# Kernel optimization log

Hardware: AMD Instinct MI355X
Metric: run time of the kernel (lower is better)

## Reference

```python
import jax, jax.numpy as jnp
import numpy as np

EPS = 1e-5
NUM_HEADS = 16
NUM_KV_HEADS = 4
HEAD_DIM = 64
TOP_K = 2


def _layer_norm(x, w, b):
    m = jnp.mean(x, axis=-1, keepdims=True)
    v = jnp.mean((x - m) ** 2, axis=-1, keepdims=True)
    return (x - m) * jax.lax.rsqrt(v + EPS) * w + b


def setup_inputs() -> dict:
    key = jax.random.key(0)
    ks = jax.random.split(key, 8)
    S, B, H = 2048, 1, 1024
    E, F = 8, 4096
    q_per_kv = NUM_HEADS // NUM_KV_HEADS
    qkv_out = NUM_KV_HEADS * (q_per_kv + 2) * HEAD_DIM  # 1536

    def w(k, shape, scale=0.02):
        return jax.random.normal(k, shape, dtype=jnp.float32) * scale

    return {
        "hidden_states": jax.random.normal(ks[0], (S, B, H), dtype=jnp.float32),
        "ln1_weight": jnp.ones((H,), jnp.float32),
        "ln1_bias": jnp.zeros((H,), jnp.float32),
        "ln2_weight": jnp.ones((H,), jnp.float32),
        "ln2_bias": jnp.zeros((H,), jnp.float32),
        "qkv_weight": w(ks[1], (qkv_out, H)),
        "proj_weight": w(ks[2], (H, H)),
        "router_weight": w(ks[3], (H, E)),
        "moe_w1": w(ks[4], (E, H, F)),
        "moe_w2": w(ks[5], (E, F, H)),
    }


def reference(hidden_states, ln1_weight, ln1_bias, ln2_weight, ln2_bias,
              qkv_weight, proj_weight, router_weight, moe_w1, moe_w2):
    S, B, H = hidden_states.shape
    D = HEAD_DIM
    Hq, Hkv = NUM_HEADS, NUM_KV_HEADS
    g = Hq // Hkv                      # queries per kv head (GQA group)
    scale = 1.0 / np.sqrt(D)

    # ---- attention block ----
    ln1_out = _layer_norm(hidden_states, ln1_weight, ln1_bias)
    qkv = ln1_out @ qkv_weight.T                      # [S,B,Hkv*(g+2)*D]
    qkv = qkv.reshape(S, B, Hkv, (g + 2) * D)
    q = qkv[..., : g * D].reshape(S, B, Hq, D)        # [S,B,Hq,D]
    k = qkv[..., g * D : (g + 1) * D]                 # [S,B,Hkv,D]
    v = qkv[..., (g + 1) * D :]                       # [S,B,Hkv,D]

    # cp_size == 1 -> Ulysses all-to-alls are identity
    q_bf = q.transpose(1, 2, 0, 3).reshape(B, Hkv, g, S, D)  # [B,Hkv,g,S,D]
    k_bf = k.transpose(1, 2, 0, 3)                           # [B,Hkv,S,D]
    v_bf = v.transpose(1, 2, 0, 3)

    scores = jnp.einsum("bkgsd,bktd->bkgst", q_bf, k_bf) * scale
    causal = jnp.tril(jnp.ones((S, S), dtype=bool))
    scores = jnp.where(causal, scores, jnp.float32(-1e30))
    probs = jax.nn.softmax(scores, axis=-1)
    attn = jnp.einsum("bkgst,bktd->bkgsd", probs, v_bf)      # [B,Hkv,g,S,D]
    attn = attn.reshape(B, Hq, S, D).transpose(2, 0, 1, 3).reshape(S, B, Hq * D)

    proj_out = attn @ proj_weight.T
    hidden_after_attn = hidden_states + proj_out

    # ---- MoE block ----
    ln2_out = _layer_norm(hidden_after_attn, ln2_weight, ln2_bias)
    x = ln2_out.reshape(-1, H)                        # [T,H]
    T = x.shape[0]

    logits = x @ router_weight                        # [T,E] (fp32)
    rprobs = jax.nn.softmax(logits, axis=-1)
    top_p, top_i = jax.lax.top_k(rprobs, TOP_K)       # [T,k]
    top_p = top_p / jnp.sum(top_p, axis=-1, keepdims=True)

    # ep_size == 1: dispatch/sort/all-to-all are a pure permutation; compute
    # each expert densely over all tokens, then gather the routed outputs
    # (identical math to sort+grouped-GEMM+unsort).
    fc1 = jnp.einsum("th,ehf->etf", x, moe_w1)        # [E,T,F]
    act = jax.nn.gelu(fc1, approximate=False)
    y = jnp.einsum("etf,efh->eth", act, moe_w2)       # [E,T,H]

    tok = jnp.arange(T)[:, None]                      # [T,1]
    gathered = y[top_i, tok, :]                       # [T,k,H]
    moe_out = jnp.sum(gathered * top_p[..., None], axis=1)  # [T,H]

    return hidden_after_attn + moe_out.reshape(S, B, H)
```

## Files before the change

kernel.cpp:

```cpp
#include <hip/hip_runtime.h>
#include <cstdint>
#include <cstddef>

typedef unsigned short u16;
typedef __attribute__((ext_vector_type(8))) short bf16x8;
typedef __attribute__((ext_vector_type(4))) float f32x4;

#define MFMA16(a, b, c) __builtin_amdgcn_mfma_f32_16x16x32_bf16((a), (b), (c), 0, 0, 0)

__device__ __forceinline__ u16 f2bf(float f) {
  uint32_t u = __builtin_bit_cast(uint32_t, f);
  u += 0x7fffu + ((u >> 16) & 1u);
  return (u16)(u >> 16);
}
__device__ __forceinline__ float bf2f(u16 h) {
  uint32_t u = ((uint32_t)h) << 16;
  return __builtin_bit_cast(float, u);
}

__device__ __forceinline__ void gload_lds16(const void* g, void* l) {
  __builtin_amdgcn_global_load_lds(
      (const __attribute__((address_space(1))) uint32_t*)g,
      (__attribute__((address_space(3))) uint32_t*)l, 16, 0, 0);
}

template<bool WRITE_LO, bool WRITE_F32>
__launch_bounds__(256)
__global__ void ln_kernel(const float* __restrict__ in,
                          const float* __restrict__ w, const float* __restrict__ b,
                          u16* __restrict__ out_hi, u16* __restrict__ out_lo,
                          float* __restrict__ out_f32)
{
  int row = blockIdx.x;
  int tid = threadIdx.x;
  const float* x = in + (size_t)row * 1024;
  float4 v = *(const float4*)(x + tid * 4);
  float s  = v.x + v.y + v.z + v.w;
  float s2 = v.x*v.x + v.y*v.y + v.z*v.z + v.w*v.w;
  #pragma unroll
  for (int d = 1; d < 64; d <<= 1) { s += __shfl_xor(s, d); s2 += __shfl_xor(s2, d); }
  __shared__ float red[2][4];
  int wid = tid >> 6;
  if ((tid & 63) == 0) { red[0][wid] = s; red[1][wid] = s2; }
  __syncthreads();
  s  = red[0][0] + red[0][1] + red[0][2] + red[0][3];
  s2 = red[1][0] + red[1][1] + red[1][2] + red[1][3];
  float mean = s * (1.0f / 1024.0f);
  float var  = s2 * (1.0f / 1024.0f) - mean * mean;
  float rstd = rsqrtf(var + 1e-5f);
  float vv[4] = {v.x, v.y, v.z, v.w};
  #pragma unroll
  for (int j = 0; j < 4; ++j) {
    int c = tid * 4 + j;
    float y = (vv[j] - mean) * rstd * w[c] + b[c];
    size_t idx = (size_t)row * 1024 + c;
    u16 hb = f2bf(y);
    out_hi[idx] = hb;
    if (WRITE_LO)  out_lo[idx] = f2bf(y - bf2f(hb));
    if (WRITE_F32) out_f32[idx] = y;
  }
}

__global__ void convert_split_kernel(const float* __restrict__ in,
                                     u16* __restrict__ hi, u16* __restrict__ lo, int n4)
{
  int i = blockIdx.x * blockDim.x + threadIdx.x;
  if (i >= n4) return;
  float4 v = *(const float4*)(in + (size_t)i * 4);
  float a[4] = {v.x, v.y, v.z, v.w};
  u16 hh[4], ll[4];
  #pragma unroll
  for (int j = 0; j < 4; ++j) {
    hh[j] = f2bf(a[j]);
    ll[j] = f2bf(a[j] - bf2f(hh[j]));
  }
  uint2 hp, lp;
  hp.x = (uint32_t)hh[0] | ((uint32_t)hh[1] << 16);
  hp.y = (uint32_t)hh[2] | ((uint32_t)hh[3] << 16);
  lp.x = (uint32_t)ll[0] | ((uint32_t)ll[1] << 16);
  lp.y = (uint32_t)ll[2] | ((uint32_t)ll[3] << 16);
  *(uint2*)(hi + (size_t)i * 4) = hp;
  *(uint2*)(lo + (size_t)i * 4) = lp;
}

__global__ void transpose_convert_kernel(const float* __restrict__ in, u16* __restrict__ out,
                                         int R, int C)
{
  __shared__ float t[32][33];
  size_t ebase = (size_t)blockIdx.z * R * C;
  int c0 = blockIdx.x * 32, r0 = blockIdx.y * 32;
  int tx = threadIdx.x, ty = threadIdx.y;
  #pragma unroll
  for (int i = 0; i < 4; ++i)
    t[ty + 8*i][tx] = in[ebase + (size_t)(r0 + ty + 8*i) * C + (c0 + tx)];
  __syncthreads();
  #pragma unroll
  for (int i = 0; i < 4; ++i)
    out[ebase + (size_t)(c0 + ty + 8*i) * R + (r0 + tx)] = f2bf(t[tx][ty + 8*i]);
}

__global__ void vtrans_kernel(const u16* __restrict__ qkv, u16* __restrict__ vT)
{
  __shared__ u16 t[32][34];
  int kvh = blockIdx.z;
  int s0 = blockIdx.x * 32, d0 = blockIdx.y * 32;
  int tx = threadIdx.x, ty = threadIdx.y;
  #pragma unroll
  for (int i = 0; i < 4; ++i)
    t[ty + 8*i][tx] = qkv[(size_t)(s0 + ty + 8*i) * 1536 + kvh * 384 + 320 + d0 + tx];
  __syncthreads();
  #pragma unroll
  for (int i = 0; i < 4; ++i)
    vT[((size_t)kvh * 64 + d0 + ty + 8*i) * 2048 + (s0 + tx)] = t[tx][ty + 8*i];
}

template<int MODE, bool SPLIT>
__launch_bounds__(256, SPLIT ? 2 : 4)
__global__ void gemm_kernel(const u16* __restrict__ Ahi, const u16* __restrict__ Alo,
                            const u16* __restrict__ Bhi, const u16* __restrict__ Blo,
                            int N, int K,
                            u16* __restrict__ Cb_hi, u16* __restrict__ Cb_lo,
                            float* __restrict__ Cf, const float* __restrict__ resid,
                            const int* __restrict__ tok_of_pair,
                            const int* __restrict__ counts, const int* __restrict__ prefix)
{
  int bn = blockIdx.x, bm = blockIdx.y;
  int row_base = 0;
  int count = 1 << 30;
  int kbeg = 0, kend = K;
  if constexpr (MODE >= 2) {
    int e = blockIdx.z;
    count = counts[e];
    if (bm * 128 >= count) return;
    row_base = prefix[e];
    Bhi += (size_t)e * N * K;
  }
  if constexpr (MODE == 3) {
    int s = bn >> 3;
    bn &= 7;
    int kc = K >> 2;
    kbeg = s * kc; kend = kbeg + kc;
    Cf += (size_t)s * 4096 * 1024;
  }
  __shared__ u16 As[2][SPLIT ? 2 : 1][128 * 32];
  __shared__ u16 Bs[2][SPLIT ? 2 : 1][128 * 32];

  int tid = threadIdx.x;
  int lane = tid & 63;
  int lo16 = lane & 15, hi4 = lane >> 4;
  int wid = tid >> 6, wr = wid >> 1, wc = wid & 1;

  const u16* gA[2][2];
  const u16* gB[2][2];
  int eidx[2];
  #pragma unroll
  for (int q = 0; q < 2; ++q) {
    int el = (q * 256 + tid) * 8;
    int r = el >> 5, c = el & 31;
    eidx[q] = el;
    if constexpr (MODE == 2) {
      int lim = count - bm * 128 - 1;
      int lr = r < lim ? r : lim;
      int token = tok_of_pair[row_base + bm * 128 + lr];
      gA[q][0] = Ahi + (size_t)token * K + c;
    } else if constexpr (MODE == 3) {
      int lim = count - bm * 128 - 1;
      int lr = r < lim ? r : lim;
      gA[q][0] = Ahi + (size_t)(row_base + bm * 128 + lr) * K + c;
    } else {
      gA[q][0] = Ahi + (size_t)(bm * 128 + r) * K + c;
      if constexpr (SPLIT) gA[q][1] = Alo + (size_t)(bm * 128 + r) * K + c;
    }
    gB[q][0] = Bhi + (size_t)(bn * 128 + r) * K + c;
    if constexpr (SPLIT) gB[q][1] = Blo + (size_t)(bn * 128 + r) * K + c;
  }

  auto stage = [&](int buf, int k0) {
    #pragma unroll
    for (int q = 0; q < 2; ++q) {
      gload_lds16(gA[q][0] + k0, &As[buf][0][eidx[q]]);
      gload_lds16(gB[q][0] + k0, &Bs[buf][0][eidx[q]]);
      if constexpr (SPLIT) {
        gload_lds16(gA[q][1] + k0, &As[buf][1][eidx[q]]);
        gload_lds16(gB[q][1] + k0, &Bs[buf][1][eidx[q]]);
      }
    }
  };

  const f32x4 zf = {0.f, 0.f, 0.f, 0.f};
  f32x4 acc[4][4];
  #pragma unroll
  for (int m = 0; m < 4; ++m)
    #pragma unroll
    for (int n = 0; n < 4; ++n) acc[m][n] = zf;

  stage(0, kbeg);
  __syncthreads();

  int cur = 0;
  for (int k0 = kbeg; k0 < kend; k0 += 32, cur ^= 1) {
    if (k0 + 32 < kend) stage(cur ^ 1, k0 + 32);

    bf16x8 a0[4], b0[4], a1[4], b1[4];
    #pragma unroll
    for (int m = 0; m < 4; ++m)
      a0[m] = *(const bf16x8*)&As[cur][0][(wr * 64 + m * 16 + lo16) * 32 + hi4 * 8];
    #pragma unroll
    for (int n = 0; n < 4; ++n)
      b0[n] = *(const bf16x8*)&Bs[cur][0][(wc * 64 + n * 16 + lo16) * 32 + hi4 * 8];
    if constexpr (SPLIT) {
      #pragma unroll
      for (int m = 0; m < 4; ++m)
        a1[m] = *(const bf16x8*)&As[cur][1][(wr * 64 + m * 16 + lo16) * 32 + hi4 * 8];
      #pragma unroll
      for (int n = 0; n < 4; ++n)
        b1[n] = *(const bf16x8*)&Bs[cur][1][(wc * 64 + n * 16 + lo16) * 32 + hi4 * 8];
    }
    #pragma unroll
    for (int m = 0; m < 4; ++m)
      #pragma unroll
      for (int n = 0; n < 4; ++n) {
        acc[m][n] = MFMA16(a0[m], b0[n], acc[m][n]);
        if constexpr (SPLIT) {
          acc[m][n] = MFMA16(a0[m], b1[n], acc[m][n]);
          acc[m][n] = MFMA16(a1[m], b0[n], acc[m][n]);
        }
      }
    __syncthreads();
  }

  #pragma unroll
  for (int m = 0; m < 4; ++m)
    #pragma unroll
    for (int n = 0; n < 4; ++n)
      #pragma unroll
      for (int r = 0; r < 4; ++r) {
        int lr = wr * 64 + m * 16 + hi4 * 4 + r;
        int col = bn * 128 + wc * 64 + n * 16 + lo16;
        float v = acc[m][n][r];
        if constexpr (MODE == 0) {
          size_t idx = (size_t)(bm * 128 + lr) * N + col;
          u16 hb = f2bf(v);
          Cb_hi[idx] = hb;
          Cb_lo[idx] = f2bf(v - bf2f(hb));
        } else if constexpr (MODE == 1) {
          size_t idx = (size_t)(bm * 128 + lr) * N + col;
          Cf[idx] = v + resid[idx];
        } else if constexpr (MODE == 2) {
          if (bm * 128 + lr < count) {
            size_t idx = (size_t)(row_base + bm * 128 + lr) * N + col;
            float g = 0.5f * v * (1.0f + erff(v * 0.70710678118654752f));
            Cb_hi[idx] = f2bf(g);
          }
        } else {
          if (bm * 128 + lr < count) {
            size_t idx = (size_t)(row_base + bm * 128 + lr) * N + col;
            Cf[idx] = v;
          }
        }
      }
}

struct QState {
  bf16x8 qf[2][2];
  f32x4 o[4];
  float m_r[4], l_r[4];
  int qrow[4];
};

__device__ __forceinline__ void qstate_init(QState& S,
    const u16* qkv_hi, const u16* qkv_lo, int q0w, int qoff, int lo16, int hi4)
{
  const u16* ph = qkv_hi + (size_t)(q0w + lo16) * 1536 + qoff + hi4 * 8;
  const u16* pl = qkv_lo + (size_t)(q0w + lo16) * 1536 + qoff + hi4 * 8;
  S.qf[0][0] = *(const bf16x8*)ph;  S.qf[0][1] = *(const bf16x8*)(ph + 32);
  S.qf[1][0] = *(const bf16x8*)pl;  S.qf[1][1] = *(const bf16x8*)(pl + 32);
  const f32x4 zf = {0.f, 0.f, 0.f, 0.f};
  #pragma unroll
  for (int r = 0; r < 4; ++r) { S.m_r[r] = -INFINITY; S.l_r[r] = 0.f; S.qrow[r] = q0w + hi4 * 4 + r; }
  #pragma unroll
  for (int n = 0; n < 4; ++n) S.o[n] = zf;
}

__device__ __forceinline__ void attn_tile(QState& S, int kv0,
    const u16* Ks0, const u16* Ks1, const u16* Vs0, const u16* Vs1,
    u16* Ps0, u16* Ps1, int lo16, int hi4)
{
  const f32x4 zf = {0.f, 0.f, 0.f, 0.f};
  f32x4 sc[4];
  __builtin_amdgcn_s_setprio(1);
  #pragma unroll
  for (int c2 = 0; c2 < 4; ++c2) {
    sc[c2] = zf;
    int krow = c2 * 16 + lo16;
    const u16* kb  = &Ks0[krow * 64];
    const u16* kbl = &Ks1[krow * 64];
    bf16x8 kh0 = *(const bf16x8*)&kb [((hi4    ) ^ (krow & 7)) * 8];
    bf16x8 kh1 = *(const bf16x8*)&kb [((hi4 + 4) ^ (krow & 7)) * 8];
    bf16x8 kl0 = *(const bf16x8*)&kbl[((hi4    ) ^ (krow & 7)) * 8];
    bf16x8 kl1 = *(const bf16x8*)&kbl[((hi4 + 4) ^ (krow & 7)) * 8];
    sc[c2] = MFMA16(S.qf[0][0], kh0, sc[c2]);
    sc[c2] = MFMA16(S.qf[0][1], kh1, sc[c2]);
    sc[c2] = MFMA16(S.qf[0][0], kl0, sc[c2]);
    sc[c2] = MFMA16(S.qf[0][1], kl1, sc[c2]);
    sc[c2] = MFMA16(S.qf[1][0], kh0, sc[c2]);
    sc[c2] = MFMA16(S.qf[1][1], kh1, sc[c2]);
  }
  __builtin_amdgcn_s_setprio(0);

  float tmax[4] = {-INFINITY, -INFINITY, -INFINITY, -INFINITY};
  #pragma unroll
  for (int c2 = 0; c2 < 4; ++c2) {
    int kv = kv0 + c2 * 16 + lo16;
    #pragma unroll
    for (int r = 0; r < 4; ++r) {
      float sv = sc[c2][r] * 0.125f;
      if (kv > S.qrow[r]) sv = -1e30f;
      sc[c2][r] = sv;
      tmax[r] = fmaxf(tmax[r], sv);
    }
  }
  #pragma unroll
  for (int d = 1; d < 16; d <<= 1)
    #pragma unroll
    for (int r = 0; r < 4; ++r)
      tmax[r] = fmaxf(tmax[r], __shfl_xor(tmax[r], d));
  float rs[4], rowsum[4];
  #pragma unroll
  for (int r = 0; r < 4; ++r) {
    float mn = fmaxf(S.m_r[r], tmax[r]);
    rs[r] = __expf(S.m_r[r] - mn);
    S.m_r[r] = mn;
    rowsum[r] = 0.f;
  }
  #pragma unroll
  for (int c2 = 0; c2 < 4; ++c2)
    #pragma unroll
    for (int r = 0; r < 4; ++r) {
      float pv = __expf(sc[c2][r] - S.m_r[r]);
      sc[c2][r] = pv;
      rowsum[r] += pv;
    }
  #pragma unroll
  for (int d = 1; d < 16; d <<= 1)
    #pragma unroll
    for (int r = 0; r < 4; ++r)
      rowsum[r] += __shfl_xor(rowsum[r], d);
  #pragma unroll
  for (int r = 0; r < 4; ++r) S.l_r[r] = S.l_r[r] * rs[r] + rowsum[r];
  #pragma unroll
  for (int n = 0; n < 4; ++n)
    #pragma unroll
    for (int r = 0; r < 4; ++r) S.o[n][r] *= rs[r];

  #pragma unroll
  for (int c2 = 0; c2 < 4; ++c2)
    #pragma unroll
    for (int r = 0; r < 4; ++r) {
      float pv = sc[c2][r];
      u16 ph = f2bf(pv);
      int pidx = (hi4 * 4 + r) * 72 + c2 * 16 + lo16;
      Ps0[pidx] = ph;
      Ps1[pidx] = f2bf(pv - bf2f(ph));
    }

  __builtin_amdgcn_s_setprio(1);
  #pragma unroll
  for (int k2 = 0; k2 < 2; ++k2) {
    bf16x8 pah = *(const bf16x8*)&Ps0[lo16 * 72 + k2 * 32 + hi4 * 8];
    bf16x8 pal = *(const bf16x8*)&Ps1[lo16 * 72 + k2 * 32 + hi4 * 8];
    #pragma unroll
    for (int n = 0; n < 4; ++n) {
      int vrow = n * 16 + lo16;
      bf16x8 vh = *(const bf16x8*)&Vs0[vrow * 64 + (((k2 * 4 + hi4) ^ (vrow & 7))) * 8];
      bf16x8 vl = *(const bf16x8*)&Vs1[vrow * 64 + (((k2 * 4 + hi4) ^ (vrow & 7))) * 8];
      S.o[n] = MFMA16(pah, vh, S.o[n]);
      S.o[n] = MFMA16(pah, vl, S.o[n]);
      S.o[n] = MFMA16(pal, vh, S.o[n]);
    }
  }
  __builtin_amdgcn_s_setprio(0);
}

__device__ __forceinline__ void qstate_out(QState& S, int q0w, int h,
    u16* out_hi, u16* out_lo, int lo16, int hi4)
{
  #pragma unroll
  for (int n = 0; n < 4; ++n)
    #pragma unroll
    for (int r = 0; r < 4; ++r) {
      float v = S.o[n][r] / S.l_r[r];
      size_t idx = (size_t)(q0w + hi4 * 4 + r) * 1024 + h * 64 + n * 16 + lo16;
      u16 hb = f2bf(v);
      out_hi[idx] = hb;
      out_lo[idx] = f2bf(v - bf2f(hb));
    }
}

__launch_bounds__(256)
__global__ void attn_kernel(const u16* __restrict__ qkv_hi, const u16* __restrict__ qkv_lo,
                            const u16* __restrict__ vT_hi, const u16* __restrict__ vT_lo,
                            u16* __restrict__ out_hi, u16* __restrict__ out_lo)
{
  int id = blockIdx.y * 32 + blockIdx.x;
  int h = id & 15;
  int j = (id >> 4) & 15;
  int qb = (id < 256) ? (31 - j) : j;
  int kvh = h >> 2, gi = h & 3;
  int tid = threadIdx.x;
  int lane = tid & 63;
  int w = tid >> 6;
  int lo16 = lane & 15, hi4 = lane >> 4;
  int q0w = qb * 64 + w * 16;
  int qoff = kvh * 384 + gi * 64;
  int koff = kvh * 384 + 256;

  __shared__ u16 Ks[2][64 * 64];
  __shared__ u16 Vs[2][64 * 64];
  __shared__ u16 Ps[2][4][16 * 72];
  u16* Ps0 = &Ps[0][w][0];
  u16* Ps1 = &Ps[1][w][0];

  QState S;
  qstate_init(S, qkv_hi, qkv_lo, q0w, qoff, lo16, hi4);

  for (int t = 0; t <= qb; ++t) {
    int kv0 = t * 64;
    __syncthreads();
    #pragma unroll
    for (int it = 0; it < 2; ++it) {
      int u = it * 256 + tid;
      int row = u >> 3, ch = u & 7;
      int d = (ch ^ (row & 7)) * 8;
      *(uint4*)&Ks[0][row * 64 + d] = *(const uint4*)(qkv_hi + (size_t)(kv0 + row) * 1536 + koff + ch * 8);
      *(uint4*)&Ks[1][row * 64 + d] = *(const uint4*)(qkv_lo + (size_t)(kv0 + row) * 1536 + koff + ch * 8);
      *(uint4*)&Vs[0][row * 64 + d] = *(const uint4*)(vT_hi + ((size_t)kvh * 64 + row) * 2048 + kv0 + ch * 8);
      *(uint4*)&Vs[1][row * 64 + d] = *(const uint4*)(vT_lo + ((size_t)kvh * 64 + row) * 2048 + kv0 + ch * 8);
    }
    __syncthreads();

    attn_tile(S, kv0, Ks[0], Ks[1], Vs[0], Vs[1], Ps0, Ps1, lo16, hi4);
  }

  qstate_out(S, q0w, h, out_hi, out_lo, lo16, hi4);
}

__launch_bounds__(64)
__global__ void router_kernel(const float* __restrict__ x, const float* __restrict__ rw,
                              int* __restrict__ counts, int* __restrict__ esel,
                              int* __restrict__ slotsel, float* __restrict__ wsel)
{
  int t = blockIdx.x;
  int l = threadIdx.x;
  float acc[8] = {0.f, 0.f, 0.f, 0.f, 0.f, 0.f, 0.f, 0.f};
  const float* xr = x + (size_t)t * 1024;
  for (int hh = l; hh < 1024; hh += 64) {
    float xv = xr[hh];
    const float* wp = rw + hh * 8;
    #pragma unroll
    for (int e = 0; e < 8; ++e) acc[e] = fmaf(xv, wp[e], acc[e]);
  }
  #pragma unroll
  for (int e = 0; e < 8; ++e)
    #pragma unroll
    for (int d = 1; d < 64; d <<= 1) acc[e] += __shfl_xor(acc[e], d);
  if (l == 0) {
    int e1 = 0;
    #pragma unroll
    for (int e = 1; e < 8; ++e) if (acc[e] > acc[e1]) e1 = e;
    int e2 = -1;
    #pragma unroll
    for (int e = 0; e < 8; ++e) {
      if (e == e1) continue;
      if (e2 < 0 || acc[e] > acc[e2]) e2 = e;
    }
    float p1 = 1.0f / (1.0f + expf(acc[e2] - acc[e1]));
    float p2 = 1.0f - p1;
    int s1 = atomicAdd(&counts[e1], 1);
    int s2 = atomicAdd(&counts[e2], 1);
    esel[t * 2] = e1; esel[t * 2 + 1] = e2;
    slotsel[t * 2] = s1; slotsel[t * 2 + 1] = s2;
    wsel[t * 2] = p1; wsel[t * 2 + 1] = p2;
  }
}

__global__ void build_lists_kernel(const int* __restrict__ counts, int* __restrict__ prefix,
                                   const int* __restrict__ esel, const int* __restrict__ slotsel,
                                   int* __restrict__ tok_of_pair, int* __restrict__ pair_idx)
{
  __shared__ int pfx[8];
  if (threadIdx.x == 0) {
    int a = 0;
    for (int e = 0; e < 8; ++e) { pfx[e] = a; prefix[e] = a; a += counts[e]; }
  }
  __syncthreads();
  for (int t = threadIdx.x; t < 2048; t += 256) {
    #pragma unroll
    for (int k = 0; k < 2; ++k) {
      int e = esel[t * 2 + k];
      int row = pfx[e] + slotsel[t * 2 + k];
      tok_of_pair[row] = t;
      pair_idx[t * 2 + k] = row;
    }
  }
}

__launch_bounds__(256)
__global__ void final_kernel(const float* __restrict__ hattn, const float* __restrict__ y,
                             const int* __restrict__ pair_idx, const float* __restrict__ wsel,
                             float* __restrict__ out)
{
  int t = blockIdx.x;
  int c = threadIdx.x * 4;
  int p0 = pair_idx[t * 2], p1 = pair_idx[t * 2 + 1];
  float w0 = wsel[t * 2], w1 = wsel[t * 2 + 1];
  float4 a = *(const float4*)(hattn + (size_t)t * 1024 + c);
  float y0x = 0.f, y0y = 0.f, y0z = 0.f, y0w = 0.f;
  float y1x = 0.f, y1y = 0.f, y1z = 0.f, y1w = 0.f;
  #pragma unroll
  for (int s = 0; s < 4; ++s) {
    const float* base = y + (size_t)s * 4096 * 1024;
    float4 v0 = *(const float4*)(base + (size_t)p0 * 1024 + c);
    float4 v1 = *(const float4*)(base + (size_t)p1 * 1024 + c);
    y0x += v0.x; y0y += v0.y; y0z += v0.z; y0w += v0.w;
    y1x += v1.x; y1y += v1.y; y1z += v1.z; y1w += v1.w;
  }
  float4 r;
  r.x = a.x + w0 * y0x + w1 * y1x;
  r.y = a.y + w0 * y0y + w1 * y1y;
  r.z = a.z + w0 * y0z + w1 * y1z;
  r.w = a.w + w0 * y0w + w1 * y1w;
  *(float4*)(out + (size_t)t * 1024 + c) = r;
}

extern "C" void kernel_launch(void* const* d_in, const int* in_sizes, int n_in,
                              void* d_out, int out_size, void* d_ws, size_t ws_size,
                              hipStream_t stream)
{
  const float* hidden   = (const float*)d_in[0];
  const float* ln1_w    = (const float*)d_in[1];
  const float* ln1_b    = (const float*)d_in[2];
  const float* ln2_w    = (const float*)d_in[3];
  const float* ln2_b    = (const float*)d_in[4];
  const float* qkv_w    = (const float*)d_in[5];
  const float* proj_w   = (const float*)d_in[6];
  const float* router_w = (const float*)d_in[7];
  const float* moe_w1   = (const float*)d_in[8];
  const float* moe_w2   = (const float*)d_in[9];
  float* out = (float*)d_out;

  char* ws = (char*)d_ws;
  size_t off = 0;
  auto alloc = [&](size_t bytes) -> void* {
    void* p = (void*)(ws + off);
    off += (bytes + 255) & ~(size_t)255;
    return p;
  };

  u16* wT      = (u16*)alloc(8ull * 4096 * 1024 * 2);
  float* hattn = (float*)alloc(2048ull * 1024 * 4);
  u16* x_hi    = (u16*)alloc(2048ull * 1024 * 2);
  u16* act     = (u16*)alloc(4096ull * 4096 * 2);
  float* ybuf  = (float*)alloc(4ull * 4096 * 1024 * 4);

  char* ov = (char*)ybuf;
  size_t oo = 0;
  auto oalloc = [&](size_t bytes) -> void* {
    void* p = (void*)(ov + oo);
    oo += (bytes + 255) & ~(size_t)255;
    return p;
  };
  u16* ln1_hi  = (u16*)oalloc(2048ull * 1024 * 2);
  u16* ln1_lo  = (u16*)oalloc(2048ull * 1024 * 2);
  u16* qw_hi   = (u16*)oalloc(1536ull * 1024 * 2);
  u16* qw_lo   = (u16*)oalloc(1536ull * 1024 * 2);
  u16* pw_hi   = (u16*)oalloc(1024ull * 1024 * 2);
  u16* pw_lo   = (u16*)oalloc(1024ull * 1024 * 2);
  u16* qkv_hi  = (u16*)oalloc(2048ull * 1536 * 2);
  u16* qkv_lo  = (u16*)oalloc(2048ull * 1536 * 2);
  u16* vt_hi   = (u16*)oalloc(4ull * 64 * 2048 * 2);
  u16* vt_lo   = (u16*)oalloc(4ull * 64 * 2048 * 2);
  u16* at_hi   = (u16*)oalloc(2048ull * 1024 * 2);
  u16* at_lo   = (u16*)oalloc(2048ull * 1024 * 2);
  float* x_f32 = (float*)oalloc(2048ull * 1024 * 4);

  int* counts  = (int*)alloc(8 * 4);
  int* prefix  = (int*)alloc(8 * 4);
  int* esel    = (int*)alloc(2048ull * 2 * 4);
  int* slotsel = (int*)alloc(2048ull * 2 * 4);
  int* topair  = (int*)alloc(4096ull * 4);
  int* pairidx = (int*)alloc(2048ull * 2 * 4);
  float* wsel  = (float*)alloc(2048ull * 2 * 4);

  hipMemsetAsync(counts, 0, 8 * 4, stream);

  ln_kernel<true, false><<<2048, 256, 0, stream>>>(hidden, ln1_w, ln1_b, ln1_hi, ln1_lo, nullptr);

  convert_split_kernel<<<1536, 256, 0, stream>>>(qkv_w, qw_hi, qw_lo, 1536 * 1024 / 4);
  convert_split_kernel<<<1024, 256, 0, stream>>>(proj_w, pw_hi, pw_lo, 1024 * 1024 / 4);

  gemm_kernel<0, true><<<dim3(12, 16, 1), 256, 0, stream>>>(
      ln1_hi, ln1_lo, qw_hi, qw_lo, 1536, 1024,
      qkv_hi, qkv_lo, nullptr, nullptr, nullptr, nullptr, nullptr);

  vtrans_kernel<<<dim3(64, 2, 4), dim3(32, 8), 0, stream>>>(qkv_hi, vt_hi);
  vtrans_kernel<<<dim3(64, 2, 4), dim3(32, 8), 0, stream>>>(qkv_lo, vt_lo);

  attn_kernel<<<dim3(32, 16), 256, 0, stream>>>(qkv_hi, qkv_lo, vt_hi, vt_lo, at_hi, at_lo);

  gemm_kernel<1, true><<<dim3(8, 16, 1), 256, 0, stream>>>(
      at_hi, at_lo, pw_hi, pw_lo, 1024, 1024,
      nullptr, nullptr, hattn, hidden, nullptr, nullptr, nullptr);

  ln_kernel<false, true><<<2048, 256, 0, stream>>>(hattn, ln2_w, ln2_b, x_hi, nullptr, x_f32);

  router_kernel<<<2048, 64, 0, stream>>>(x_f32, router_w, counts, esel, slotsel, wsel);
  build_lists_kernel<<<1, 256, 0, stream>>>(counts, prefix, esel, slotsel, topair, pairidx);

  transpose_convert_kernel<<<dim3(128, 32, 8), dim3(32, 8), 0, stream>>>(moe_w1, wT, 1024, 4096);

  gemm_kernel<2, false><<<dim3(32, 16, 8), 256, 0, stream>>>(
      x_hi, nullptr, wT, nullptr, 4096, 1024,
      act, nullptr, nullptr, nullptr, topair, counts, prefix);

  transpose_convert_kernel<<<dim3(32, 128, 8), dim3(32, 8), 0, stream>>>(moe_w2, wT, 4096, 1024);

  gemm_kernel<3, false><<<dim3(32, 16, 8), 256, 0, stream>>>(
      act, nullptr, wT, nullptr, 1024, 4096,
      nullptr, nullptr, ybuf, nullptr, topair, counts, prefix);

  final_kernel<<<2048, 256, 0, stream>>>(hattn, ybuf, pairidx, wsel, out);
}
```

Measured before the change: 503.9 us.

## Add 256x256-tile MoE grouped GEMM kernel with swizzled LDS and 512 threads

Moves the two MoE expert GEMMs (fc1 with gathered tokens plus GELU, and the split-K fc2) from the 128x128 generic kernel to a new 256x256-tile kernel with 8 waves, 64-wide K steps and an XOR-swizzled LDS layout meant to avoid bank conflicts. The grid is reordered so the expert index is the fastest-varying block dimension. The larger tiles raise data reuse per block and halve the number of K iterations, but use more LDS and registers per block and waste more rows when an expert's token count is not a multiple of 256. The old generic kernel is reduced to the split-precision modes used by the attention GEMMs.

```diff
diff --git a/kernel.cpp b/kernel.cpp
--- a/kernel.cpp
+++ b/kernel.cpp
@@ -114,36 +114,17 @@
     vT[((size_t)kvh * 64 + d0 + ty + 8*i) * 2048 + (s0 + tx)] = t[tx][ty + 8*i];
 }
 
-template<int MODE, bool SPLIT>
-__launch_bounds__(256, SPLIT ? 2 : 4)
+template<int MODE>
+__launch_bounds__(256, 2)
 __global__ void gemm_kernel(const u16* __restrict__ Ahi, const u16* __restrict__ Alo,
                             const u16* __restrict__ Bhi, const u16* __restrict__ Blo,
                             int N, int K,
                             u16* __restrict__ Cb_hi, u16* __restrict__ Cb_lo,
-                            float* __restrict__ Cf, const float* __restrict__ resid,
-                            const int* __restrict__ tok_of_pair,
-                            const int* __restrict__ counts, const int* __restrict__ prefix)
+                            float* __restrict__ Cf, const float* __restrict__ resid)
 {
   int bn = blockIdx.x, bm = blockIdx.y;
-  int row_base = 0;
-  int count = 1 << 30;
-  int kbeg = 0, kend = K;
-  if constexpr (MODE >= 2) {
-    int e = blockIdx.z;
-    count = counts[e];
-    if (bm * 128 >= count) return;
-    row_base = prefix[e];
-    Bhi += (size_t)e * N * K;
-  }
-  if constexpr (MODE == 3) {
-    int s = bn >> 3;
-    bn &= 7;
-    int kc = K >> 2;
-    kbeg = s * kc; kend = kbeg + kc;
-    Cf += (size_t)s * 4096 * 1024;
-  }
-  __shared__ u16 As[2][SPLIT ? 2 : 1][128 * 32];
-  __shared__ u16 Bs[2][SPLIT ? 2 : 1][128 * 32];
+  __shared__ u16 As[2][2][128 * 32];
+  __shared__ u16 Bs[2][2][128 * 32];
 
   int tid = threadIdx.x;
   int lane = tid & 63;
@@ -158,21 +139,10 @@
     int el = (q * 256 + tid) * 8;
     int r = el >> 5, c = el & 31;
     eidx[q] = el;
-    if constexpr (MODE == 2) {
-      int lim = count - bm * 128 - 1;
-      int lr = r < lim ? r : lim;
-      int token = tok_of_pair[row_base + bm * 128 + lr];
-      gA[q][0] = Ahi + (size_t)token * K + c;
-    } else if constexpr (MODE == 3) {
-      int lim = count - bm * 128 - 1;
-      int lr = r < lim ? r : lim;
-      gA[q][0] = Ahi + (size_t)(row_base + bm * 128 + lr) * K + c;
-    } else {
-      gA[q][0] = Ahi + (size_t)(bm * 128 + r) * K + c;
-      if constexpr (SPLIT) gA[q][1] = Alo + (size_t)(bm * 128 + r) * K + c;
-    }
+    gA[q][0] = Ahi + (size_t)(bm * 128 + r) * K + c;
+    gA[q][1] = Alo + (size_t)(bm * 128 + r) * K + c;
     gB[q][0] = Bhi + (size_t)(bn * 128 + r) * K + c;
-    if constexpr (SPLIT) gB[q][1] = Blo + (size_t)(bn * 128 + r) * K + c;
+    gB[q][1] = Blo + (size_t)(bn * 128 + r) * K + c;
   }
 
   auto stage = [&](int buf, int k0) {
@@ -180,10 +150,8 @@
     for (int q = 0; q < 2; ++q) {
       gload_lds16(gA[q][0] + k0, &As[buf][0][eidx[q]]);
       gload_lds16(gB[q][0] + k0, &Bs[buf][0][eidx[q]]);
-      if constexpr (SPLIT) {
-        gload_lds16(gA[q][1] + k0, &As[buf][1][eidx[q]]);
-        gload_lds16(gB[q][1] + k0, &Bs[buf][1][eidx[q]]);
-      }
+      gload_lds16(gA[q][1] + k0, &As[buf][1][eidx[q]]);
+      gload_lds16(gB[q][1] + k0, &Bs[buf][1][eidx[q]]);
     }
   };
 
@@ -194,12 +162,11 @@
     #pragma unroll
     for (int n = 0; n < 4; ++n) acc[m][n] = zf;
 
-  stage(0, kbeg);
+  stage(0, 0);
   __syncthreads();
-
   int cur = 0;
-  for (int k0 = kbeg; k0 < kend; k0 += 32, cur ^= 1) {
-    if (k0 + 32 < kend) stage(cur ^ 1, k0 + 32);
+  for (int k0 = 0; k0 < K; k0 += 32, cur ^= 1) {
+    if (k0 + 32 < K) stage(cur ^ 1, k0 + 32);
 
     bf16x8 a0[4], b0[4], a1[4], b1[4];
     #pragma unroll
@@ -208,23 +175,19 @@
     #pragma unroll
     for (int n = 0; n < 4; ++n)
       b0[n] = *(const bf16x8*)&Bs[cur][0][(wc * 64 + n * 16 + lo16) * 32 + hi4 * 8];
-    if constexpr (SPLIT) {
-      #pragma unroll
-      for (int m = 0; m < 4; ++m)
-        a1[m] = *(const bf16x8*)&As[cur][1][(wr * 64 + m * 16 + lo16) * 32 + hi4 * 8];
-      #pragma unroll
-      for (int n = 0; n < 4; ++n)
-        b1[n] = *(const bf16x8*)&Bs[cur][1][(wc * 64 + n * 16 + lo16) * 32 + hi4 * 8];
-    }
+    #pragma unroll
+    for (int m = 0; m < 4; ++m)
+      a1[m] = *(const bf16x8*)&As[cur][1][(wr * 64 + m * 16 + lo16) * 32 + hi4 * 8];
+    #pragma unroll
+    for (int n = 0; n < 4; ++n)
+      b1[n] = *(const bf16x8*)&Bs[cur][1][(wc * 64 + n * 16 + lo16) * 32 + hi4 * 8];
     #pragma unroll
     for (int m = 0; m < 4; ++m)
       #pragma unroll
       for (int n = 0; n < 4; ++n) {
         acc[m][n] = MFMA16(a0[m], b0[n], acc[m][n]);
-        if constexpr (SPLIT) {
-          acc[m][n] = MFMA16(a0[m], b1[n], acc[m][n]);
-          acc[m][n] = MFMA16(a1[m], b0[n], acc[m][n]);
-        }
+        acc[m][n] = MFMA16(a0[m], b1[n], acc[m][n]);
+        acc[m][n] = MFMA16(a1[m], b0[n], acc[m][n]);
       }
     __syncthreads();
   }
@@ -238,23 +201,135 @@
         int lr = wr * 64 + m * 16 + hi4 * 4 + r;
         int col = bn * 128 + wc * 64 + n * 16 + lo16;
         float v = acc[m][n][r];
+        size_t idx = (size_t)(bm * 128 + lr) * N + col;
         if constexpr (MODE == 0) {
-          size_t idx = (size_t)(bm * 128 + lr) * N + col;
           u16 hb = f2bf(v);
           Cb_hi[idx] = hb;
           Cb_lo[idx] = f2bf(v - bf2f(hb));
-        } else if constexpr (MODE == 1) {
-          size_t idx = (size_t)(bm * 128 + lr) * N + col;
+        } else {
           Cf[idx] = v + resid[idx];
-        } else if constexpr (MODE == 2) {
-          if (bm * 128 + lr < count) {
-            size_t idx = (size_t)(row_base + bm * 128 + lr) * N + col;
+        }
+      }
+}
+
+template<int MODE>
+__launch_bounds__(512, 2)
+__global__ void gemm256_kernel(const u16* __restrict__ A, const u16* __restrict__ B,
+                               int N, int K,
+                               u16* __restrict__ Cb, float* __restrict__ Cf,
+                               const int* __restrict__ tok_of_pair,
+                               const int* __restrict__ counts, const int* __restrict__ prefix)
+{
+  int e = blockIdx.x;
+  int bn = blockIdx.y;
+  int bm, kbeg = 0, kend = K;
+  if constexpr (MODE == 2) {
+    bm = blockIdx.z;
+  } else {
+    bm = blockIdx.z & 3;
+    int s = blockIdx.z >> 2;
+    int kc = K >> 2;
+    kbeg = s * kc; kend = kbeg + kc;
+    Cf += (size_t)s * 4096 * 1024;
+  }
+  int count = counts[e];
+  if (bm * 256 >= count) return;
+  int row_base = prefix[e];
+  B += (size_t)e * N * K;
+
+  __shared__ u16 As[2][256 * 64];
+  __shared__ u16 Bs[2][256 * 64];
+
+  int tid = threadIdx.x;
+  int lane = tid & 63;
+  int wid = tid >> 6;
+  int lo16 = lane & 15, hi4 = lane >> 4;
+  int wr = wid >> 2, wc = wid & 3;
+
+  const u16* gA[4];
+  const u16* gB[4];
+  int dstc[4];
+  int lim = count - bm * 256 - 1;
+  #pragma unroll
+  for (int q = 0; q < 4; ++q) {
+    int c = q * 512 + tid;
+    int r = c >> 3;
+    int kc8 = (c & 7) ^ (r & 7);
+    dstc[q] = c * 8;
+    int lr = r < lim ? r : lim;
+    if constexpr (MODE == 2) {
+      int token = tok_of_pair[row_base + bm * 256 + lr];
+      gA[q] = A + (size_t)token * K + kc8 * 8;
+    } else {
+      gA[q] = A + (size_t)(row_base + bm * 256 + lr) * K + kc8 * 8;
+    }
+    gB[q] = B + (size_t)(bn * 256 + r) * K + kc8 * 8;
+  }
+
+  auto stage = [&](int buf, int k0) {
+    #pragma unroll
+    for (int q = 0; q < 4; ++q) {
+      gload_lds16(gA[q] + k0, &As[buf][dstc[q]]);
+      gload_lds16(gB[q] + k0, &Bs[buf][dstc[q]]);
+    }
+  };
+
+  const f32x4 zf = {0.f, 0.f, 0.f, 0.f};
+  f32x4 acc[8][4];
+  #pragma unroll
+  for (int m = 0; m < 8; ++m)
+    #pragma unroll
+    for (int n = 0; n < 4; ++n) acc[m][n] = zf;
+
+  int nt = (kend - kbeg) >> 6;
+  stage(0, kbeg);
+  asm volatile("s_waitcnt vmcnt(0)" ::: "memory");
+  __builtin_amdgcn_s_barrier();
+
+  int cur = 0;
+  for (int t = 0; t < nt; ++t) {
+    if (t + 1 < nt) stage(cur ^ 1, kbeg + (t + 1) * 64);
+
+    #pragma unroll
+    for (int ks = 0; ks < 2; ++ks) {
+      bf16x8 a[8], b[4];
+      #pragma unroll
+      for (int m = 0; m < 8; ++m) {
+        int row = wr * 128 + m * 16 + lo16;
+        a[m] = *(const bf16x8*)&As[cur][row * 64 + (((ks * 4 + hi4) ^ (row & 7)) * 8)];
+      }
+      #pragma unroll
+      for (int n = 0; n < 4; ++n) {
+        int row = wc * 64 + n * 16 + lo16;
+        b[n] = *(const bf16x8*)&Bs[cur][row * 64 + (((ks * 4 + hi4) ^ (row & 7)) * 8)];
+      }
+      #pragma unroll
+      for (int m = 0; m < 8; ++m)
+        #pragma unroll
+        for (int n = 0; n < 4; ++n)
+          acc[m][n] = MFMA16(a[m], b[n], acc[m][n]);
+    }
+
+    asm volatile("s_waitcnt vmcnt(0)" ::: "memory");
+    __builtin_amdgcn_s_barrier();
+    cur ^= 1;
+  }
+
+  #pragma unroll
+  for (int m = 0; m < 8; ++m)
+    #pragma unroll
+    for (int n = 0; n < 4; ++n)
+      #pragma unroll
+      for (int r = 0; r < 4; ++r) {
+        int rig = bm * 256 + wr * 128 + m * 16 + hi4 * 4 + r;
+        if (rig < count) {
+          int col = bn * 256 + wc * 64 + n * 16 + lo16;
+          size_t idx = (size_t)(row_base + rig) * N + col;
+          float v = acc[m][n][r];
+          if constexpr (MODE == 2) {
             float g = 0.5f * v * (1.0f + erff(v * 0.70710678118654752f));
-            Cb_hi[idx] = f2bf(g);
-          }
-        } else {
-          if (bm * 128 + lr < count) {
-            size_t idx = (size_t)(row_base + bm * 128 + lr) * N + col;
+            Cb[idx] = f2bf(g);
+          } else {
             Cf[idx] = v;
           }
         }
@@ -599,18 +674,18 @@
   convert_split_kernel<<<1536, 256, 0, stream>>>(qkv_w, qw_hi, qw_lo, 1536 * 1024 / 4);
   convert_split_kernel<<<1024, 256, 0, stream>>>(proj_w, pw_hi, pw_lo, 1024 * 1024 / 4);
 
-  gemm_kernel<0, true><<<dim3(12, 16, 1), 256, 0, stream>>>(
+  gemm_kernel<0><<<dim3(12, 16, 1), 256, 0, stream>>>(
       ln1_hi, ln1_lo, qw_hi, qw_lo, 1536, 1024,
-      qkv_hi, qkv_lo, nullptr, nullptr, nullptr, nullptr, nullptr);
+      qkv_hi, qkv_lo, nullptr, nullptr);
 
   vtrans_kernel<<<dim3(64, 2, 4), dim3(32, 8), 0, stream>>>(qkv_hi, vt_hi);
   vtrans_kernel<<<dim3(64, 2, 4), dim3(32, 8), 0, stream>>>(qkv_lo, vt_lo);
 
   attn_kernel<<<dim3(32, 16), 256, 0, stream>>>(qkv_hi, qkv_lo, vt_hi, vt_lo, at_hi, at_lo);
 
-  gemm_kernel<1, true><<<dim3(8, 16, 1), 256, 0, stream>>>(
+  gemm_kernel<1><<<dim3(8, 16, 1), 256, 0, stream>>>(
       at_hi, at_lo, pw_hi, pw_lo, 1024, 1024,
-      nullptr, nullptr, hattn, hidden, nullptr, nullptr, nullptr);
+      nullptr, nullptr, hattn, hidden);
 
   ln_kernel<false, true><<<2048, 256, 0, stream>>>(hattn, ln2_w, ln2_b, x_hi, nullptr, x_f32);
 
@@ -619,15 +694,13 @@
 
   transpose_convert_kernel<<<dim3(128, 32, 8), dim3(32, 8), 0, stream>>>(moe_w1, wT, 1024, 4096);
 
-  gemm_kernel<2, false><<<dim3(32, 16, 8), 256, 0, stream>>>(
-      x_hi, nullptr, wT, nullptr, 4096, 1024,
-      act, nullptr, nullptr, nullptr, topair, counts, prefix);
+  gemm256_kernel<2><<<dim3(8, 16, 4), 512, 0, stream>>>(
+      x_hi, wT, 4096, 1024, act, nullptr, topair, counts, prefix);
 
   transpose_convert_kernel<<<dim3(32, 128, 8), dim3(32, 8), 0, stream>>>(moe_w2, wT, 4096, 1024);
 
-  gemm_kernel<3, false><<<dim3(32, 16, 8), 256, 0, stream>>>(
-      act, nullptr, wT, nullptr, 1024, 4096,
-      nullptr, nullptr, ybuf, nullptr, topair, counts, prefix);
+  gemm256_kernel<3><<<dim3(8, 4, 16), 512, 0, stream>>>(
+      act, wT, 1024, 4096, nullptr, ybuf, topair, counts, prefix);
 
   final_kernel<<<2048, 256, 0, stream>>>(hattn, ybuf, pairidx, wsel, out);
 }
```

Measured after the change: 524.4 us. +4.1%, slower.
